# Kernel tuning notes

Measured on AMD Instinct MI355X. Metric: run time of the kernel, lower is better.

The kernel has to match this reference:

```python
import jax, jax.numpy as jnp
import numpy as np
from jax import lax

TAU = 2.0
VTH = 1.0
T = 4

def heaviside(x):
    return (x >= 0.0).astype(x.dtype)

def lif_step(v, x):
    # decay_input=False, v_reset=0: v <- v*(1-1/tau) + x ; hard reset to 0
    v = v * (1.0 - 1.0 / TAU) + x
    s = heaviside(v - VTH)
    v = v * (1.0 - s)
    return v, s

def setup_inputs() -> dict:
    key = jax.random.key(0)
    k = jax.random.split(key, 5)
    B, H, W3, W4 = 128, 64, 8, 32
    cc, N, O = 8, 512, 16
    flat = cc * H * W3 * W4  # 131072
    x = jax.random.normal(k[0], (B, 2, H, W3, W4), dtype=jnp.float32)
    w_conv = jax.random.normal(k[1], (cc, 2, 3, 3), dtype=jnp.float32) / np.sqrt(2 * 9)
    w1 = jax.random.normal(k[2], (N, flat), dtype=jnp.float32) / np.sqrt(flat)
    w2 = jax.random.normal(k[3], (N, N), dtype=jnp.float32) / np.sqrt(N)
    w_out = jax.random.normal(k[4], (O, N), dtype=jnp.float32) / np.sqrt(N)
    return {"x": x, "w_conv": w_conv, "w1": w1, "w2": w2, "w_out": w_out}

def reference(x, w_conv, w1, w2, w_out):
    B = x.shape[0]
    # input.reshape(B, C, -1, W4)
    xr = x.reshape(B, x.shape[1], -1, x.shape[4])  # (B, 2, 512, 32)
    conv_input = lax.conv_general_dilated(
        xr, w_conv, window_strides=(1, 1), padding="SAME",
        dimension_numbers=("NCHW", "OIHW", "NCHW"))  # (B, cc, 512, 32)

    # lifconv applied T times to the same conv_input with persistent state
    def conv_step(v, _):
        return lif_step(v, conv_input)
    _, conv_spikes = lax.scan(conv_step, jnp.zeros_like(conv_input), None, length=T)  # (T,B,cc,H',W')

    N = w1.shape[0]
    def fc_step(carry, s_conv):
        v1, v2 = carry
        z1 = s_conv.reshape(B, -1) @ w1.T
        v1, s1 = lif_step(v1, z1)
        z2 = s1 @ w2.T
        v2, s2 = lif_step(v2, z2)
        return (v1, v2), (s1, s2)

    v0 = (jnp.zeros((B, N), x.dtype), jnp.zeros((B, N), x.dtype))
    _, (s1_rec, s2_rec) = lax.scan(fc_step, v0, conv_spikes)  # (T,B,N) each

    out = s2_rec.mean(axis=0) @ w_out.T  # (B, O)
    conv_spk_rec = jnp.moveaxis(conv_spikes, 0, 1)   # (B,T,cc,H',W')
    input_spk_rec = jnp.moveaxis(s1_rec, 0, 1)       # (B,T,N)
    hidden_spk_rec = jnp.moveaxis(s2_rec, 0, 1)      # (B,T,N)
    return (out, conv_spk_rec, input_spk_rec, hidden_spk_rec)
```

## Files before the change

### kernel.cpp

```cpp
#include <hip/hip_runtime.h>
#include <stdint.h>


#define OFF_CONV  2048ll
#define OFF_IN    67110912ll
#define OFF_HID   67373056ll

typedef short bf16x8 __attribute__((ext_vector_type(8)));
typedef float f32x4  __attribute__((ext_vector_type(4)));

__device__ __forceinline__ unsigned short f2bf(float f) {
  unsigned u = __float_as_uint(f);
  u += 0x7FFFu + ((u >> 16) & 1u);
  return (unsigned short)(u >> 16);
}

__device__ __forceinline__ void expand2(unsigned x, unsigned& o0, unsigned& o1) {
  o0 = (x & 1u) * 0x3F80u | (x & 0x100u) * 0x3F8000u;
  unsigned y = x >> 16;
  o1 = (y & 1u) * 0x3F80u | (y & 0x100u) * 0x3F8000u;
}

__global__ __launch_bounds__(256) void conv_lif_kernel(
    const float* __restrict__ x, const float* __restrict__ wc,
    float* __restrict__ out, unsigned char* __restrict__ patt)
{
  __shared__ float wcs[144];
  int tid = threadIdx.x;
  if (tid < 144) wcs[tid] = wc[tid];
  __syncthreads();

  int idx = blockIdx.x * 256 + tid;
  int b   = idx >> 15;
  int k4  = idx & 32767;
  int co  = k4 >> 12;
  int rem = k4 & 4095;
  int h   = rem >> 3;
  int w0  = (rem & 7) * 4;

  const float* xb = x + (long long)b * 32768;
  float c[4] = {0.f, 0.f, 0.f, 0.f};
#pragma unroll
  for (int ci = 0; ci < 2; ++ci) {
    const float* xc = xb + ci * 16384;
    const float* wk = wcs + co * 18 + ci * 9;
    float win[3][6];
#pragma unroll
    for (int r = 0; r < 3; ++r) {
      int hh = h - 1 + r;
      if (hh >= 0 && hh < 512) {
        const float* row = xc + hh * 32;
        float4 m = *(const float4*)(row + w0);
        win[r][1] = m.x; win[r][2] = m.y; win[r][3] = m.z; win[r][4] = m.w;
        win[r][0] = (w0 > 0)  ? row[w0 - 1] : 0.f;
        win[r][5] = (w0 < 28) ? row[w0 + 4] : 0.f;
      } else {
#pragma unroll
        for (int j = 0; j < 6; ++j) win[r][j] = 0.f;
      }
    }
#pragma unroll
    for (int r = 0; r < 3; ++r)
#pragma unroll
      for (int dw = 0; dw < 3; ++dw) {
        float wgt = wk[r * 3 + dw];
#pragma unroll
        for (int j = 0; j < 4; ++j) c[j] += win[r][j + dw] * wgt;
      }
  }

  int k = co * 16384 + h * 32 + w0;
  float* ob = out + OFF_CONV + (long long)b * 524288 + k;
  float v[4] = {0.f, 0.f, 0.f, 0.f};
  unsigned p[4] = {0, 0, 0, 0};
#pragma unroll
  for (int t = 0; t < 4; ++t) {
    f32x4 sv;
#pragma unroll
    for (int j = 0; j < 4; ++j) {
      v[j] = v[j] * 0.5f + c[j];
      int si = (v[j] >= 1.0f) ? 1 : 0;
      sv[j] = (float)si;
      if (si) v[j] = 0.f;
      p[j] |= (unsigned)si << t;
    }
    __builtin_nontemporal_store(sv, (f32x4*)(ob + t * 131072));
  }
  unsigned pb = p[0] | (p[1] << 8) | (p[2] << 16) | (p[3] << 24);
  *(unsigned*)(patt + (long long)b * 131072 + k) = pb;
}

__global__ __launch_bounds__(256) void transpose512(
    const float* __restrict__ w2, float* __restrict__ w2t)
{
  __shared__ float tile[32][33];
  int bx = blockIdx.x & 15, by = blockIdx.x >> 4;
  int tx = threadIdx.x & 31, ty = threadIdx.x >> 5;
#pragma unroll
  for (int i = 0; i < 32; i += 8)
    tile[ty + i][tx] = w2[(by * 32 + ty + i) * 512 + bx * 32 + tx];
  __syncthreads();
#pragma unroll
  for (int i = 0; i < 32; i += 8)
    w2t[(bx * 32 + ty + i) * 512 + by * 32 + tx] = tile[tx][ty + i];
}

__global__ __launch_bounds__(512, 2) void gemm_kernel(
    const unsigned char* __restrict__ patt, const float* __restrict__ w1,
    float* __restrict__ partials, int steps)
{
  __shared__ __attribute__((aligned(16))) unsigned short As[2][4][128][40];
  __shared__ __attribute__((aligned(16))) unsigned short Bh[2][128][40];
  __shared__ __attribute__((aligned(16))) unsigned short Bl[2][128][40];

  const int tid   = threadIdx.x;
  const int nt    = blockIdx.x & 3;
  const int chunk = blockIdx.x >> 2;
  const long long k0 = (long long)chunk * steps * 32;

  const int r  = tid >> 2;
  const int ko = (tid & 3) * 8;

  const unsigned char* pA = patt + (long long)r * 131072 + k0 + ko;
  const float* pB = w1 + (long long)(nt * 128 + r) * 131072 + k0 + ko;

  const int lane = tid & 63;
  const int wid  = tid >> 6;
  const int t    = wid >> 1;
  const int nh   = wid & 1;
  const int l15 = lane & 15, quad = lane >> 4;

  f32x4 acc[8][4];
#pragma unroll
  for (int i = 0; i < 8; ++i)
#pragma unroll
    for (int j = 0; j < 4; ++j) acc[i][j] = (f32x4){0.f, 0.f, 0.f, 0.f};

  uint2  pa = *(const uint2*)(pA);
  float4 f0 = *(const float4*)(pB + 0);
  float4 f1 = *(const float4*)(pB + 4);

  for (int s = 0; s < steps; ++s) {
    const int buf = s & 1;

    uint2 pan = pa; float4 f0n = f0, f1n = f1;
    if (s + 1 < steps) {
      pan = *(const uint2*)(pA + (s + 1) * 32);
      f0n = *(const float4*)(pB + (s + 1) * 32);
      f1n = *(const float4*)(pB + (s + 1) * 32 + 4);
    }

#pragma unroll
    for (int tt = 0; tt < 4; ++tt) {
      unsigned x0 = (pa.x >> tt) & 0x01010101u;
      unsigned x1 = (pa.y >> tt) & 0x01010101u;
      unsigned o0, o1, o2, o3;
      expand2(x0, o0, o1);
      expand2(x1, o2, o3);
      *(uint4*)&As[buf][tt][r][ko] = make_uint4(o0, o1, o2, o3);
    }

    float fv[8] = {f0.x, f0.y, f0.z, f0.w, f1.x, f1.y, f1.z, f1.w};
    unsigned hp[4], lp[4];
#pragma unroll
    for (int i = 0; i < 4; ++i) {
      unsigned short h0 = f2bf(fv[2 * i]);
      unsigned short h1 = f2bf(fv[2 * i + 1]);
      float r0 = fv[2 * i]     - __uint_as_float((unsigned)h0 << 16);
      float r1 = fv[2 * i + 1] - __uint_as_float((unsigned)h1 << 16);
      hp[i] = (unsigned)h0 | ((unsigned)h1 << 16);
      lp[i] = (unsigned)f2bf(r0) | ((unsigned)f2bf(r1) << 16);
    }
    *(uint4*)&Bh[buf][r][ko] = make_uint4(hp[0], hp[1], hp[2], hp[3]);
    *(uint4*)&Bl[buf][r][ko] = make_uint4(lp[0], lp[1], lp[2], lp[3]);

    __syncthreads();

    bf16x8 a[8], bh[4], bl[4];
#pragma unroll
    for (int f = 0; f < 8; ++f)
      a[f] = *(const bf16x8*)&As[buf][t][f * 16 + l15][quad * 8];
#pragma unroll
    for (int f = 0; f < 4; ++f) {
      bh[f] = *(const bf16x8*)&Bh[buf][nh * 64 + f * 16 + l15][quad * 8];
      bl[f] = *(const bf16x8*)&Bl[buf][nh * 64 + f * 16 + l15][quad * 8];
    }
    __builtin_amdgcn_s_setprio(1);
#pragma unroll
    for (int fm = 0; fm < 8; ++fm)
#pragma unroll
      for (int fn = 0; fn < 4; ++fn) {
        acc[fm][fn] = __builtin_amdgcn_mfma_f32_16x16x32_bf16(a[fm], bh[fn], acc[fm][fn], 0, 0, 0);
        acc[fm][fn] = __builtin_amdgcn_mfma_f32_16x16x32_bf16(a[fm], bl[fn], acc[fm][fn], 0, 0, 0);
      }
    __builtin_amdgcn_s_setprio(0);

    pa = pan; f0 = f0n; f1 = f1n;
  }

  float* pc = partials + (long long)chunk * 262144;
#pragma unroll
  for (int fm = 0; fm < 8; ++fm)
#pragma unroll
    for (int fn = 0; fn < 4; ++fn) {
      int m = t * 128 + fm * 16 + quad * 4;
      int n = nt * 128 + nh * 64 + fn * 16 + l15;
#pragma unroll
      for (int rg = 0; rg < 4; ++rg)
        pc[(long long)(m + rg) * 512 + n] = acc[fm][fn][rg];
    }
}

__global__ __launch_bounds__(256) void reduce_kernel(
    const float* __restrict__ partials, float* __restrict__ z1, int S)
{
  int idx = (blockIdx.x * 256 + threadIdx.x) * 4;
  float4 a = {0.f, 0.f, 0.f, 0.f};
  for (int c = 0; c < S; ++c) {
    float4 p = *(const float4*)(partials + (long long)c * 262144 + idx);
    a.x += p.x; a.y += p.y; a.z += p.z; a.w += p.w;
  }
  *(float4*)(z1 + idx) = a;
}

__global__ __launch_bounds__(512) void fc_kernel(
    const float* __restrict__ z1, const float* __restrict__ w2t,
    const float* __restrict__ wout, float* __restrict__ out)
{
  int b = blockIdx.x;
  int n = threadIdx.x;
  __shared__ float s1s[512];
  __shared__ float red[512];
  __shared__ unsigned short idxs[512];
  __shared__ int cnts[8];

  const int wid = n >> 6, lane = n & 63;

  float v1 = 0.f, v2 = 0.f, ssum = 0.f;
#pragma unroll
  for (int t = 0; t < 4; ++t) {
    float z = z1[((t * 128 + b) << 9) + n];
    v1 = v1 * 0.5f + z;
    float s1 = (v1 >= 1.0f) ? 1.f : 0.f;
    out[OFF_IN + ((long long)b * 4 + t) * 512 + n] = s1;
    if (s1 != 0.f) v1 = 0.f;

    unsigned long long m = __ballot(s1 != 0.f);
    if (lane == 0) cnts[wid] = __popcll(m);
    __syncthreads();
    int base = 0, total = 0;
#pragma unroll
    for (int w = 0; w < 8; ++w) {
      int c = cnts[w];
      base  += (w < wid) ? c : 0;
      total += c;
    }
    if (s1 != 0.f) {
      int pos = base + (int)__popcll(m & ((1ull << lane) - 1ull));
      idxs[pos] = (unsigned short)n;
    }
    __syncthreads();

    float z2 = 0.f;
    int j = 0;
    for (; j + 8 <= total; j += 8) {
      float a0 = w2t[((int)idxs[j + 0] << 9) + n];
      float a1 = w2t[((int)idxs[j + 1] << 9) + n];
      float a2 = w2t[((int)idxs[j + 2] << 9) + n];
      float a3 = w2t[((int)idxs[j + 3] << 9) + n];
      float a4 = w2t[((int)idxs[j + 4] << 9) + n];
      float a5 = w2t[((int)idxs[j + 5] << 9) + n];
      float a6 = w2t[((int)idxs[j + 6] << 9) + n];
      float a7 = w2t[((int)idxs[j + 7] << 9) + n];
      z2 += a0; z2 += a1; z2 += a2; z2 += a3;
      z2 += a4; z2 += a5; z2 += a6; z2 += a7;
    }
    for (; j < total; ++j)
      z2 += w2t[((int)idxs[j] << 9) + n];

    v2 = v2 * 0.5f + z2;
    float s2 = (v2 >= 1.0f) ? 1.f : 0.f;
    out[OFF_HID + ((long long)b * 4 + t) * 512 + n] = s2;
    if (s2 != 0.f) v2 = 0.f;
    ssum += s2;
    __syncthreads();
  }

  s1s[n] = ssum * 0.25f;
  __syncthreads();

  int o = n & 15, part = n >> 4;
  float p = 0.f;
#pragma unroll
  for (int j = 0; j < 16; ++j)
    p += s1s[part * 16 + j] * wout[o * 512 + part * 16 + j];
  red[n] = p;
  __syncthreads();
  if (n < 16) {
    float a = 0.f;
#pragma unroll
    for (int pp = 0; pp < 32; ++pp) a += red[pp * 16 + n];
    out[b * 16 + n] = a;
  }
}

extern "C" void kernel_launch(void* const* d_in, const int* in_sizes, int n_in,
                              void* d_out, int out_size, void* d_ws, size_t ws_size,
                              hipStream_t stream) {
  const float* x     = (const float*)d_in[0];
  const float* wconv = (const float*)d_in[1];
  const float* w1    = (const float*)d_in[2];
  const float* w2    = (const float*)d_in[3];
  const float* wout  = (const float*)d_in[4];
  float* out = (float*)d_out;
  char* ws = (char*)d_ws;

  unsigned char* patt = (unsigned char*)ws;
  float* w2t      = (float*)(ws + 16777216);
  float* z1       = (float*)(ws + 16777216 + 1048576);
  float* partials = (float*)(ws + 16777216 + 2097152);

  int S = 64;
  while (S > 1 && (size_t)(18874368ull + (size_t)S * 1048576ull) > ws_size) S >>= 1;
  int steps = 4096 / S;

  hipLaunchKernelGGL(conv_lif_kernel, dim3(16384), dim3(256), 0, stream,
                     x, wconv, out, patt);
  hipLaunchKernelGGL(transpose512, dim3(256), dim3(256), 0, stream, w2, w2t);
  hipLaunchKernelGGL(gemm_kernel, dim3(4 * S), dim3(512), 0, stream,
                     patt, w1, partials, steps);
  hipLaunchKernelGGL(reduce_kernel, dim3(256), dim3(256), 0, stream,
                     partials, z1, S);
  hipLaunchKernelGGL(fc_kernel, dim3(128), dim3(512), 0, stream,
                     z1, w2t, wout, out);
}
```

Before: 579.7 us.

## Software-pipeline GEMM staging, remap block order, fuse split-K reduce into FC

Restructures the split-K GEMM main loop so global loads run two steps ahead and the LDS staging of the next tile is interleaved between two halves of the MFMA work, with one barrier per step instead of storing then computing. Block-to-tile mapping changes so consecutive blocks share the same N tile across K chunks. The separate reduce kernel is removed and the FC kernel sums the split-K partials directly, saving a launch and a z1 round trip. This adds register pressure for the extra prefetch buffers, and the FC kernel now does strided reads over S partials per element.

```diff
diff --git a/kernel.cpp b/kernel.cpp
--- a/kernel.cpp
+++ b/kernel.cpp
@@ -114,8 +114,9 @@
   __shared__ __attribute__((aligned(16))) unsigned short Bl[2][128][40];
 
   const int tid   = threadIdx.x;
-  const int nt    = blockIdx.x & 3;
-  const int chunk = blockIdx.x >> 2;
+  const int S     = gridDim.x >> 2;
+  const int nt    = blockIdx.x / S;
+  const int chunk = blockIdx.x - nt * S;
   const long long k0 = (long long)chunk * steps * 32;
 
   const int r  = tid >> 2;
@@ -136,67 +137,100 @@
 #pragma unroll
     for (int j = 0; j < 4; ++j) acc[i][j] = (f32x4){0.f, 0.f, 0.f, 0.f};
 
-  uint2  pa = *(const uint2*)(pA);
-  float4 f0 = *(const float4*)(pB + 0);
-  float4 f1 = *(const float4*)(pB + 4);
+  uint2  pa[2];  float4 f0[2], f1[2];
+
+#define STAGE(bb, PP, F0, F1)                                              \
+  {                                                                        \
+    _Pragma("unroll")                                                      \
+    for (int tt = 0; tt < 4; ++tt) {                                       \
+      unsigned x0 = ((PP).x >> tt) & 0x01010101u;                          \
+      unsigned x1 = ((PP).y >> tt) & 0x01010101u;                          \
+      unsigned o0, o1, o2, o3;                                             \
+      expand2(x0, o0, o1);                                                 \
+      expand2(x1, o2, o3);                                                 \
+      *(uint4*)&As[bb][tt][r][ko] = make_uint4(o0, o1, o2, o3);            \
+    }                                                                      \
+    float fv[8] = {(F0).x, (F0).y, (F0).z, (F0).w,                         \
+                   (F1).x, (F1).y, (F1).z, (F1).w};                        \
+    unsigned hp[4], lp[4];                                                 \
+    _Pragma("unroll")                                                      \
+    for (int i = 0; i < 4; ++i) {                                          \
+      unsigned short h0 = f2bf(fv[2 * i]);                                 \
+      unsigned short h1 = f2bf(fv[2 * i + 1]);                             \
+      float r0 = fv[2 * i]     - __uint_as_float((unsigned)h0 << 16);      \
+      float r1 = fv[2 * i + 1] - __uint_as_float((unsigned)h1 << 16);      \
+      hp[i] = (unsigned)h0 | ((unsigned)h1 << 16);                         \
+      lp[i] = (unsigned)f2bf(r0) | ((unsigned)f2bf(r1) << 16);             \
+    }                                                                      \
+    *(uint4*)&Bh[bb][r][ko] = make_uint4(hp[0], hp[1], hp[2], hp[3]);      \
+    *(uint4*)&Bl[bb][r][ko] = make_uint4(lp[0], lp[1], lp[2], lp[3]);      \
+  }
+
+  pa[0] = *(const uint2*)(pA);
+  f0[0] = *(const float4*)(pB + 0);
+  f1[0] = *(const float4*)(pB + 4);
+  if (steps > 1) {
+    pa[1] = *(const uint2*)(pA + 32);
+    f0[1] = *(const float4*)(pB + 32);
+    f1[1] = *(const float4*)(pB + 36);
+  }
+  STAGE(0, pa[0], f0[0], f1[0]);
+  __syncthreads();
 
   for (int s = 0; s < steps; ++s) {
     const int buf = s & 1;
-
-    uint2 pan = pa; float4 f0n = f0, f1n = f1;
-    if (s + 1 < steps) {
-      pan = *(const uint2*)(pA + (s + 1) * 32);
-      f0n = *(const float4*)(pB + (s + 1) * 32);
-      f1n = *(const float4*)(pB + (s + 1) * 32 + 4);
-    }
-
-#pragma unroll
-    for (int tt = 0; tt < 4; ++tt) {
-      unsigned x0 = (pa.x >> tt) & 0x01010101u;
-      unsigned x1 = (pa.y >> tt) & 0x01010101u;
-      unsigned o0, o1, o2, o3;
-      expand2(x0, o0, o1);
-      expand2(x1, o2, o3);
-      *(uint4*)&As[buf][tt][r][ko] = make_uint4(o0, o1, o2, o3);
-    }
-
-    float fv[8] = {f0.x, f0.y, f0.z, f0.w, f1.x, f1.y, f1.z, f1.w};
-    unsigned hp[4], lp[4];
-#pragma unroll
-    for (int i = 0; i < 4; ++i) {
-      unsigned short h0 = f2bf(fv[2 * i]);
-      unsigned short h1 = f2bf(fv[2 * i + 1]);
-      float r0 = fv[2 * i]     - __uint_as_float((unsigned)h0 << 16);
-      float r1 = fv[2 * i + 1] - __uint_as_float((unsigned)h1 << 16);
-      hp[i] = (unsigned)h0 | ((unsigned)h1 << 16);
-      lp[i] = (unsigned)f2bf(r0) | ((unsigned)f2bf(r1) << 16);
-    }
-    *(uint4*)&Bh[buf][r][ko] = make_uint4(hp[0], hp[1], hp[2], hp[3]);
-    *(uint4*)&Bl[buf][r][ko] = make_uint4(lp[0], lp[1], lp[2], lp[3]);
-
-    __syncthreads();
-
-    bf16x8 a[8], bh[4], bl[4];
-#pragma unroll
-    for (int f = 0; f < 8; ++f)
-      a[f] = *(const bf16x8*)&As[buf][t][f * 16 + l15][quad * 8];
+    const int nxt = (s + 1) & 1;
+
+    if (s + 2 < steps) {
+      pa[buf] = *(const uint2*)(pA + (long long)(s + 2) * 32);
+      f0[buf] = *(const float4*)(pB + (long long)(s + 2) * 32);
+      f1[buf] = *(const float4*)(pB + (long long)(s + 2) * 32 + 4);
+    }
+
+    bf16x8 bh[4], bl[4];
 #pragma unroll
     for (int f = 0; f < 4; ++f) {
       bh[f] = *(const bf16x8*)&Bh[buf][nh * 64 + f * 16 + l15][quad * 8];
       bl[f] = *(const bf16x8*)&Bl[buf][nh * 64 + f * 16 + l15][quad * 8];
     }
-    __builtin_amdgcn_s_setprio(1);
-#pragma unroll
-    for (int fm = 0; fm < 8; ++fm)
-#pragma unroll
-      for (int fn = 0; fn < 4; ++fn) {
-        acc[fm][fn] = __builtin_amdgcn_mfma_f32_16x16x32_bf16(a[fm], bh[fn], acc[fm][fn], 0, 0, 0);
-        acc[fm][fn] = __builtin_amdgcn_mfma_f32_16x16x32_bf16(a[fm], bl[fn], acc[fm][fn], 0, 0, 0);
-      }
-    __builtin_amdgcn_s_setprio(0);
-
-    pa = pan; f0 = f0n; f1 = f1n;
-  }
+
+    {
+      bf16x8 a[4];
+#pragma unroll
+      for (int f = 0; f < 4; ++f)
+        a[f] = *(const bf16x8*)&As[buf][t][f * 16 + l15][quad * 8];
+      __builtin_amdgcn_s_setprio(1);
+#pragma unroll
+      for (int fm = 0; fm < 4; ++fm)
+#pragma unroll
+        for (int fn = 0; fn < 4; ++fn) {
+          acc[fm][fn] = __builtin_amdgcn_mfma_f32_16x16x32_bf16(a[fm], bh[fn], acc[fm][fn], 0, 0, 0);
+          acc[fm][fn] = __builtin_amdgcn_mfma_f32_16x16x32_bf16(a[fm], bl[fn], acc[fm][fn], 0, 0, 0);
+        }
+      __builtin_amdgcn_s_setprio(0);
+    }
+
+    if (s + 1 < steps) STAGE(nxt, pa[nxt], f0[nxt], f1[nxt]);
+
+    {
+      bf16x8 a[4];
+#pragma unroll
+      for (int f = 0; f < 4; ++f)
+        a[f] = *(const bf16x8*)&As[buf][t][64 + f * 16 + l15][quad * 8];
+      __builtin_amdgcn_s_setprio(1);
+#pragma unroll
+      for (int fm = 0; fm < 4; ++fm)
+#pragma unroll
+        for (int fn = 0; fn < 4; ++fn) {
+          acc[4 + fm][fn] = __builtin_amdgcn_mfma_f32_16x16x32_bf16(a[fm], bh[fn], acc[4 + fm][fn], 0, 0, 0);
+          acc[4 + fm][fn] = __builtin_amdgcn_mfma_f32_16x16x32_bf16(a[fm], bl[fn], acc[4 + fm][fn], 0, 0, 0);
+        }
+      __builtin_amdgcn_s_setprio(0);
+    }
+
+    __syncthreads();
+  }
+#undef STAGE
 
   float* pc = partials + (long long)chunk * 262144;
 #pragma unroll
@@ -211,21 +245,9 @@
     }
 }
 
-__global__ __launch_bounds__(256) void reduce_kernel(
-    const float* __restrict__ partials, float* __restrict__ z1, int S)
-{
-  int idx = (blockIdx.x * 256 + threadIdx.x) * 4;
-  float4 a = {0.f, 0.f, 0.f, 0.f};
-  for (int c = 0; c < S; ++c) {
-    float4 p = *(const float4*)(partials + (long long)c * 262144 + idx);
-    a.x += p.x; a.y += p.y; a.z += p.z; a.w += p.w;
-  }
-  *(float4*)(z1 + idx) = a;
-}
-
 __global__ __launch_bounds__(512) void fc_kernel(
-    const float* __restrict__ z1, const float* __restrict__ w2t,
-    const float* __restrict__ wout, float* __restrict__ out)
+    const float* __restrict__ partials, const float* __restrict__ w2t,
+    const float* __restrict__ wout, float* __restrict__ out, int S)
 {
   int b = blockIdx.x;
   int n = threadIdx.x;
@@ -239,7 +261,10 @@
   float v1 = 0.f, v2 = 0.f, ssum = 0.f;
 #pragma unroll
   for (int t = 0; t < 4; ++t) {
-    float z = z1[((t * 128 + b) << 9) + n];
+    const float* pz = partials + ((t * 128 + b) << 9) + n;
+    float z = 0.f;
+    for (int c = 0; c < S; ++c) z += pz[(long long)c * 262144];
+
     v1 = v1 * 0.5f + z;
     float s1 = (v1 >= 1.0f) ? 1.f : 0.f;
     out[OFF_IN + ((long long)b * 4 + t) * 512 + n] = s1;
@@ -317,7 +342,6 @@
 
   unsigned char* patt = (unsigned char*)ws;
   float* w2t      = (float*)(ws + 16777216);
-  float* z1       = (float*)(ws + 16777216 + 1048576);
   float* partials = (float*)(ws + 16777216 + 2097152);
 
   int S = 64;
@@ -329,8 +353,6 @@
   hipLaunchKernelGGL(transpose512, dim3(256), dim3(256), 0, stream, w2, w2t);
   hipLaunchKernelGGL(gemm_kernel, dim3(4 * S), dim3(512), 0, stream,
                      patt, w1, partials, steps);
-  hipLaunchKernelGGL(reduce_kernel, dim3(256), dim3(256), 0, stream,
-                     partials, z1, S);
   hipLaunchKernelGGL(fc_kernel, dim3(128), dim3(512), 0, stream,
-                     z1, w2t, wout, out);
-}
+                     partials, w2t, wout, out, S);
+}
```

Result: slower. 682.7 us (+17.8%).

## Shrink GEMM N-tile to 64 and single-buffer LDS to raise occupancy

Applied to the files above, without the earlier changes.

The split-K GEMM now covers 64 output columns per block instead of 128, doubling the grid to 8*S blocks. Shared memory drops to a single buffer with a second barrier per step, and the accumulators shrink to 4x4 fragments so four blocks can fit per CU. Block-to-tile mapping becomes chunk-major within each N tile, so consecutive blocks share w1 rows. The cost is that each A (spike) tile is loaded twice as often, and the extra barrier per step removes the overlap between LDS writes and MFMA work.

```diff
diff --git a/kernel.cpp b/kernel.cpp
--- a/kernel.cpp
+++ b/kernel.cpp
@@ -105,49 +105,48 @@
     w2t[(bx * 32 + ty + i) * 512 + by * 32 + tx] = tile[tx][ty + i];
 }
 
-__global__ __launch_bounds__(512, 2) void gemm_kernel(
+__global__ __launch_bounds__(512, 4) void gemm_kernel(
     const unsigned char* __restrict__ patt, const float* __restrict__ w1,
     float* __restrict__ partials, int steps)
 {
-  __shared__ __attribute__((aligned(16))) unsigned short As[2][4][128][40];
-  __shared__ __attribute__((aligned(16))) unsigned short Bh[2][128][40];
-  __shared__ __attribute__((aligned(16))) unsigned short Bl[2][128][40];
+  __shared__ __attribute__((aligned(16))) unsigned short As[4][128][40];
+  __shared__ __attribute__((aligned(16))) unsigned short Bh[64][40];
+  __shared__ __attribute__((aligned(16))) unsigned short Bl[64][40];
 
   const int tid   = threadIdx.x;
-  const int nt    = blockIdx.x & 3;
-  const int chunk = blockIdx.x >> 2;
+  const int S     = gridDim.x >> 3;
+  const int nt    = blockIdx.x / S;
+  const int chunk = blockIdx.x - nt * S;
   const long long k0 = (long long)chunk * steps * 32;
 
-  const int r  = tid >> 2;
-  const int ko = (tid & 3) * 8;
-
-  const unsigned char* pA = patt + (long long)r * 131072 + k0 + ko;
-  const float* pB = w1 + (long long)(nt * 128 + r) * 131072 + k0 + ko;
+  const int ra  = tid >> 2;
+  const int koa = (tid & 3) * 8;
+  const unsigned char* pA = patt + (long long)ra * 131072 + k0 + koa;
+
+  const int rb  = tid >> 3;
+  const int kob = (tid & 7) * 4;
+  const float* pB = w1 + (long long)(nt * 64 + rb) * 131072 + k0 + kob;
 
   const int lane = tid & 63;
   const int wid  = tid >> 6;
   const int t    = wid >> 1;
-  const int nh   = wid & 1;
+  const int mh   = wid & 1;
   const int l15 = lane & 15, quad = lane >> 4;
 
-  f32x4 acc[8][4];
-#pragma unroll
-  for (int i = 0; i < 8; ++i)
+  f32x4 acc[4][4];
+#pragma unroll
+  for (int i = 0; i < 4; ++i)
 #pragma unroll
     for (int j = 0; j < 4; ++j) acc[i][j] = (f32x4){0.f, 0.f, 0.f, 0.f};
 
-  uint2  pa = *(const uint2*)(pA);
-  float4 f0 = *(const float4*)(pB + 0);
-  float4 f1 = *(const float4*)(pB + 4);
+  uint2  pa = *(const uint2*)pA;
+  float4 fb = *(const float4*)pB;
 
   for (int s = 0; s < steps; ++s) {
-    const int buf = s & 1;
-
-    uint2 pan = pa; float4 f0n = f0, f1n = f1;
+    uint2 pan = pa; float4 fbn = fb;
     if (s + 1 < steps) {
-      pan = *(const uint2*)(pA + (s + 1) * 32);
-      f0n = *(const float4*)(pB + (s + 1) * 32);
-      f1n = *(const float4*)(pB + (s + 1) * 32 + 4);
+      pan = *(const uint2*)(pA + (long long)(s + 1) * 32);
+      fbn = *(const float4*)(pB + (long long)(s + 1) * 32);
     }
 
 #pragma unroll
@@ -157,54 +156,57 @@
       unsigned o0, o1, o2, o3;
       expand2(x0, o0, o1);
       expand2(x1, o2, o3);
-      *(uint4*)&As[buf][tt][r][ko] = make_uint4(o0, o1, o2, o3);
-    }
-
-    float fv[8] = {f0.x, f0.y, f0.z, f0.w, f1.x, f1.y, f1.z, f1.w};
-    unsigned hp[4], lp[4];
-#pragma unroll
-    for (int i = 0; i < 4; ++i) {
-      unsigned short h0 = f2bf(fv[2 * i]);
-      unsigned short h1 = f2bf(fv[2 * i + 1]);
-      float r0 = fv[2 * i]     - __uint_as_float((unsigned)h0 << 16);
-      float r1 = fv[2 * i + 1] - __uint_as_float((unsigned)h1 << 16);
-      hp[i] = (unsigned)h0 | ((unsigned)h1 << 16);
-      lp[i] = (unsigned)f2bf(r0) | ((unsigned)f2bf(r1) << 16);
-    }
-    *(uint4*)&Bh[buf][r][ko] = make_uint4(hp[0], hp[1], hp[2], hp[3]);
-    *(uint4*)&Bl[buf][r][ko] = make_uint4(lp[0], lp[1], lp[2], lp[3]);
-
-    __syncthreads();
-
-    bf16x8 a[8], bh[4], bl[4];
-#pragma unroll
-    for (int f = 0; f < 8; ++f)
-      a[f] = *(const bf16x8*)&As[buf][t][f * 16 + l15][quad * 8];
-#pragma unroll
-    for (int f = 0; f < 4; ++f) {
-      bh[f] = *(const bf16x8*)&Bh[buf][nh * 64 + f * 16 + l15][quad * 8];
-      bl[f] = *(const bf16x8*)&Bl[buf][nh * 64 + f * 16 + l15][quad * 8];
-    }
+      *(uint4*)&As[tt][ra][koa] = make_uint4(o0, o1, o2, o3);
+    }
+
+    {
+      float fv[4] = {fb.x, fb.y, fb.z, fb.w};
+      unsigned hp[2], lp[2];
+#pragma unroll
+      for (int i = 0; i < 2; ++i) {
+        unsigned short h0 = f2bf(fv[2 * i]);
+        unsigned short h1 = f2bf(fv[2 * i + 1]);
+        float r0 = fv[2 * i]     - __uint_as_float((unsigned)h0 << 16);
+        float r1 = fv[2 * i + 1] - __uint_as_float((unsigned)h1 << 16);
+        hp[i] = (unsigned)h0 | ((unsigned)h1 << 16);
+        lp[i] = (unsigned)f2bf(r0) | ((unsigned)f2bf(r1) << 16);
+      }
+      *(uint2*)&Bh[rb][kob] = make_uint2(hp[0], hp[1]);
+      *(uint2*)&Bl[rb][kob] = make_uint2(lp[0], lp[1]);
+    }
+
+    __syncthreads();
+
+    bf16x8 a[4];
+#pragma unroll
+    for (int f = 0; f < 4; ++f)
+      a[f] = *(const bf16x8*)&As[t][mh * 64 + f * 16 + l15][quad * 8];
+
     __builtin_amdgcn_s_setprio(1);
 #pragma unroll
-    for (int fm = 0; fm < 8; ++fm)
-#pragma unroll
-      for (int fn = 0; fn < 4; ++fn) {
-        acc[fm][fn] = __builtin_amdgcn_mfma_f32_16x16x32_bf16(a[fm], bh[fn], acc[fm][fn], 0, 0, 0);
-        acc[fm][fn] = __builtin_amdgcn_mfma_f32_16x16x32_bf16(a[fm], bl[fn], acc[fm][fn], 0, 0, 0);
+    for (int fn = 0; fn < 4; ++fn) {
+      bf16x8 bh = *(const bf16x8*)&Bh[fn * 16 + l15][quad * 8];
+      bf16x8 bl = *(const bf16x8*)&Bl[fn * 16 + l15][quad * 8];
+#pragma unroll
+      for (int fm = 0; fm < 4; ++fm) {
+        acc[fm][fn] = __builtin_amdgcn_mfma_f32_16x16x32_bf16(a[fm], bh, acc[fm][fn], 0, 0, 0);
+        acc[fm][fn] = __builtin_amdgcn_mfma_f32_16x16x32_bf16(a[fm], bl, acc[fm][fn], 0, 0, 0);
       }
+    }
     __builtin_amdgcn_s_setprio(0);
 
-    pa = pan; f0 = f0n; f1 = f1n;
+    __syncthreads();
+
+    pa = pan; fb = fbn;
   }
 
   float* pc = partials + (long long)chunk * 262144;
 #pragma unroll
-  for (int fm = 0; fm < 8; ++fm)
+  for (int fm = 0; fm < 4; ++fm)
 #pragma unroll
     for (int fn = 0; fn < 4; ++fn) {
-      int m = t * 128 + fm * 16 + quad * 4;
-      int n = nt * 128 + nh * 64 + fn * 16 + l15;
+      int m = t * 128 + mh * 64 + fm * 16 + quad * 4;
+      int n = nt * 64 + fn * 16 + l15;
 #pragma unroll
       for (int rg = 0; rg < 4; ++rg)
         pc[(long long)(m + rg) * 512 + n] = acc[fm][fn][rg];
@@ -327,7 +329,7 @@
   hipLaunchKernelGGL(conv_lif_kernel, dim3(16384), dim3(256), 0, stream,
                      x, wconv, out, patt);
   hipLaunchKernelGGL(transpose512, dim3(256), dim3(256), 0, stream, w2, w2t);
-  hipLaunchKernelGGL(gemm_kernel, dim3(4 * S), dim3(512), 0, stream,
+  hipLaunchKernelGGL(gemm_kernel, dim3(8 * S), dim3(512), 0, stream,
                      patt, w1, partials, steps);
   hipLaunchKernelGGL(reduce_kernel, dim3(256), dim3(256), 0, stream,
                      partials, z1, S);
```

Measured after the change: 591.3 us. 2.0% more time.
